# Optimization experiments

Hardware: AMD Instinct MI355X
Metric: run time of the kernel (lower is better)

The kernel has to match this reference:

```python
import jax, jax.numpy as jnp
import numpy as np

B, H, W, C = 4, 64, 64, 256
D = C // 8  # out_channels // queries_ratio = 32


def setup_inputs() -> dict:
    key = jax.random.key(0)
    ks = jax.random.split(key, 8)
    s_in = 1.0 / np.sqrt(C)  # he_normal-ish scale for 1x1 convs
    s_d = 1.0 / np.sqrt(D)
    return {
        "x": jax.random.normal(ks[0], (B, H, W, C), dtype=jnp.float32),
        "Wk": jax.random.normal(ks[1], (C, D), dtype=jnp.float32) * s_in,
        "bk": jnp.zeros((D,), dtype=jnp.float32),
        "Wq": jax.random.normal(ks[2], (C, D), dtype=jnp.float32) * s_in,
        "bq": jnp.zeros((D,), dtype=jnp.float32),
        "Wv": jax.random.normal(ks[3], (C, D), dtype=jnp.float32) * s_in,
        "bv": jnp.zeros((D,), dtype=jnp.float32),
        "Wo": jax.random.normal(ks[4], (D, C), dtype=jnp.float32) * s_d,
        "bo": jnp.zeros((C,), dtype=jnp.float32),
        "gamma": jax.random.normal(ks[5], (1,), dtype=jnp.float32) * 0.1,
    }


def reference(x, Wk, bk, Wq, bq, Wv, bv, Wo, bo, gamma):
    b, h, w, c = x.shape
    n = h * w
    xf = x.reshape(b, n, c)  # flatten spatial -> [B, N, C]
    # 1x1 convs == per-position channel matmuls
    k = xf @ Wk + bk  # [B, N, D]
    q = xf @ Wq + bq  # [B, N, D]
    v = xf @ Wv + bv  # [B, N, D]
    energy = jnp.einsum('bnd,bmd->bnm', q, k)  # [B, N, N] (no scaling, as in source)
    attn = jax.nn.softmax(energy, axis=-1)
    feat = jnp.einsum('bnm,bmd->bnd', attn, v)  # [B, N, D]
    out = feat @ Wo + bo  # 1x1 output conv -> [B, N, C]
    out = gamma[0] * out + xf  # gamma scale + identity shortcut (C_in == C_out)
    return out.reshape(b, h, w, c)
```

## Files before the change

kernel.cpp:

```cpp
#include <hip/hip_runtime.h>
#include <hip/hip_bf16.h>
#include <hip/hip_fp16.h>


#define BB 4
#define NN 4096
#define CC 256
#define DD 32
#define LOG2E 1.44269504088896340736f
#define THR2 11.0f
#define NROW (BB * NN)
#define KSPLIT 4
#define NCH 8

typedef _Float16 half_t;
typedef _Float16 half2_t __attribute__((ext_vector_type(2)));
typedef _Float16 half4_t __attribute__((ext_vector_type(4)));
typedef _Float16 half8_t __attribute__((ext_vector_type(8)));
typedef float f32x4 __attribute__((ext_vector_type(4)));

#define MFMA_QK(a, b, c) __builtin_amdgcn_mfma_f32_16x16x32_f16(a, b, c, 0, 0, 0)
#define MFMA_PV(a, b, c) __builtin_amdgcn_mfma_f32_16x16x16f16(a, b, c, 0, 0, 0)

static __device__ inline float fexp2(float x) {
#if __has_builtin(__builtin_amdgcn_exp2f)
    return __builtin_amdgcn_exp2f(x);
#else
    return exp2f(x);
#endif
}

__global__ __launch_bounds__(512) void proj_kernel(
    const float* __restrict__ x,
    const float* __restrict__ Wk, const float* __restrict__ bk,
    const float* __restrict__ Wq, const float* __restrict__ bq,
    const float* __restrict__ Wv, const float* __restrict__ bv,
    half_t* __restrict__ k_ws, half_t* __restrict__ q_ws, half_t* __restrict__ vT3)
{
    __shared__ half_t xs16[64][264];
    __shared__ half_t Wt[96][264];

    const int t = threadIdx.x;
    const int xcd = blockIdx.x & 7, slot = blockIdx.x >> 3;
    const int bb = xcd >> 1;
    const int c64 = (slot << 1) | (xcd & 1);
    const int row0 = bb * NN + c64 * 64;

    const float4* x4 = reinterpret_cast<const float4*>(x) + (size_t)row0 * 64;
    for (int idx = t; idx < 64 * 64; idx += 512) {
        int r = idx >> 6, c4 = idx & 63;
        float4 v = x4[r * 64 + c4];
        half4_t h;
        h[0] = (half_t)v.x; h[1] = (half_t)v.y; h[2] = (half_t)v.z; h[3] = (half_t)v.w;
        *reinterpret_cast<half4_t*>(&xs16[r][c4 * 4]) = h;
    }

    for (int idx = t; idx < 3072; idx += 512) {
        int cp = idx & 127;
        int rest = idx >> 7;
        int d4 = (rest & 7) * 4;
        int mat = rest >> 3;
        const float* Wm = (mat == 0) ? Wk : ((mat == 1) ? Wq : Wv);
        const float sc = (mat == 1) ? LOG2E : 1.0f;
        float4 w0 = *reinterpret_cast<const float4*>(Wm + (2 * cp) * DD + d4);
        float4 w1 = *reinterpret_cast<const float4*>(Wm + (2 * cp + 1) * DD + d4);
        int rbase = mat * 32 + d4;
        half2_t h;
        h[0] = (half_t)(w0.x * sc); h[1] = (half_t)(w1.x * sc);
        *reinterpret_cast<half2_t*>(&Wt[rbase + 0][2 * cp]) = h;
        h[0] = (half_t)(w0.y * sc); h[1] = (half_t)(w1.y * sc);
        *reinterpret_cast<half2_t*>(&Wt[rbase + 1][2 * cp]) = h;
        h[0] = (half_t)(w0.z * sc); h[1] = (half_t)(w1.z * sc);
        *reinterpret_cast<half2_t*>(&Wt[rbase + 2][2 * cp]) = h;
        h[0] = (half_t)(w0.w * sc); h[1] = (half_t)(w1.w * sc);
        *reinterpret_cast<half2_t*>(&Wt[rbase + 3][2 * cp]) = h;
    }
    __syncthreads();

    const int w = t >> 6, lane = t & 63;
    const int c = lane & 15, g = lane >> 4;
    const int rt = w >> 1;
    const int ct0 = (w & 1) * 3;

    f32x4 acc[3];
#pragma unroll
    for (int j = 0; j < 3; ++j) acc[j] = (f32x4){0.f, 0.f, 0.f, 0.f};

#pragma unroll
    for (int kk = 0; kk < 8; ++kk) {
        const int k0 = kk * 32 + g * 8;
        half8_t bfrag = *reinterpret_cast<const half8_t*>(&xs16[rt * 16 + c][k0]);
#pragma unroll
        for (int j = 0; j < 3; ++j) {
            half8_t afrag = *reinterpret_cast<const half8_t*>(&Wt[(ct0 + j) * 16 + c][k0]);
            acc[j] = MFMA_QK(afrag, bfrag, acc[j]);
        }
    }

    const int grow = row0 + rt * 16 + c;
#pragma unroll
    for (int j = 0; j < 3; ++j) {
        const int ct = ct0 + j;
        const int mat = ct >> 1;
        const float* bm = (mat == 0) ? bk : ((mat == 1) ? bq : bv);
        float4 bb4 = *reinterpret_cast<const float4*>(bm + (ct & 1) * 16 + g * 4);
        const int d0 = (ct & 1) * 16 + g * 4;
        if (mat < 2) {
            const float bsc = (mat == 1) ? LOG2E : 1.0f;
            half_t* dst = (mat == 0) ? k_ws : q_ws;
            half4_t h;
            h[0] = (half_t)(acc[j][0] + bb4.x * bsc);
            h[1] = (half_t)(acc[j][1] + bb4.y * bsc);
            h[2] = (half_t)(acc[j][2] + bb4.z * bsc);
            h[3] = (half_t)(acc[j][3] + bb4.w * bsc);
            *reinterpret_cast<half4_t*>(dst + (size_t)grow * DD + d0) = h;
        } else {
            const size_t tbase = (size_t)(grow >> 4) * 512;
            float vals[4] = {acc[j][0] + bb4.x, acc[j][1] + bb4.y,
                             acc[j][2] + bb4.z, acc[j][3] + bb4.w};
#pragma unroll
            for (int i = 0; i < 4; ++i) {
                int d = d0 + i;
                int l = ((c >> 2) << 4) | (d & 15);
                int h = l * 8 + ((d >> 4) << 2) + (c & 3);
                vT3[tbase + h] = (half_t)vals[i];
            }
        }
    }
}

__global__ __launch_bounds__(512) void attn_partial(
    const half_t* __restrict__ k_ws, const half_t* __restrict__ q_ws,
    const half_t* __restrict__ vT3,
    float* __restrict__ pm, float* __restrict__ ps, float* __restrict__ pO)
{
    __shared__ half_t kbuf[2][8][512];
    __shared__ half_t vbuf[2][8][512];

    const int tid = threadIdx.x;
    const int w = tid >> 6, lane = tid & 63;
    const int q = lane & 15, g = lane >> 4;
    const int xcd = blockIdx.x & 7, rest = blockIdx.x >> 3;
    const int b = xcd >> 1;
    const int u = (rest << 1) | (xcd & 1);
    const int qu = u >> 2;
    const int ks = u & 3;
    const int r0 = b * NN + qu * 256;

    half8_t qf0 = *reinterpret_cast<const half8_t*>(
        q_ws + (size_t)(r0 + (2 * w + 0) * 16 + q) * DD + g * 8);
    half8_t qf1 = *reinterpret_cast<const half8_t*>(
        q_ws + (size_t)(r0 + (2 * w + 1) * 16 + q) * DD + g * 8);

    float m0 = -3.0e38f, m1 = -3.0e38f, ss0 = 0.f, ss1 = 0.f;
    f32x4 acc00 = {0.f, 0.f, 0.f, 0.f};
    f32x4 acc01 = {0.f, 0.f, 0.f, 0.f};
    f32x4 acc10 = {0.f, 0.f, 0.f, 0.f};
    f32x4 acc11 = {0.f, 0.f, 0.f, 0.f};

    const int t0 = ks * 64;
    const half_t* ksrc = k_ws + ((size_t)b * NN + q) * DD + g * 8;
    const half_t* vsrc = vT3 + (size_t)lane * 8;

    {
        half8_t sK = *reinterpret_cast<const half8_t*>(ksrc + (size_t)(t0 + w) * 16 * DD);
        half8_t sV = *reinterpret_cast<const half8_t*>(vsrc + (size_t)(b * 256 + t0 + w) * 512);
        *reinterpret_cast<half8_t*>(&kbuf[0][w][lane * 8]) = sK;
        *reinterpret_cast<half8_t*>(&vbuf[0][w][lane * 8]) = sV;
    }
    __syncthreads();

    for (int ch = 0; ch < NCH; ++ch) {
        const int cb = ch & 1;

        half8_t sK, sV;
        if (ch + 1 < NCH) {
            const int lt = t0 + (ch + 1) * 8 + w;
            sK = *reinterpret_cast<const half8_t*>(ksrc + (size_t)lt * 16 * DD);
            sV = *reinterpret_cast<const half8_t*>(vsrc + (size_t)(b * 256 + lt) * 512);
        }

#pragma unroll
        for (int t = 0; t < 8; ++t) {
            half8_t kf = *reinterpret_cast<const half8_t*>(&kbuf[cb][t][lane * 8]);
            half8_t vv = *reinterpret_cast<const half8_t*>(&vbuf[cb][t][lane * 8]);

            f32x4 z = {0.f, 0.f, 0.f, 0.f};
            f32x4 sA = MFMA_QK(kf, qf0, z);
            f32x4 sB = MFMA_QK(kf, qf1, z);

            float tA = fmaxf(fmaxf(sA[0], sA[1]), fmaxf(sA[2], sA[3]));
            float tB = fmaxf(fmaxf(sB[0], sB[1]), fmaxf(sB[2], sB[3]));
            bool need = (tA > m0 + THR2) || (tB > m1 + THR2);
            if (__any(need)) {
                float rA = fmaxf(tA, __shfl_xor(tA, 16));
                rA = fmaxf(rA, __shfl_xor(rA, 32));
                float rB = fmaxf(tB, __shfl_xor(tB, 16));
                rB = fmaxf(rB, __shfl_xor(rB, 32));
                float n0 = fmaxf(m0, rA), n1 = fmaxf(m1, rB);
                float c0 = fexp2(m0 - n0), c1 = fexp2(m1 - n1);
                ss0 *= c0; ss1 *= c1;
                acc00 *= c0; acc01 *= c0;
                acc10 *= c1; acc11 *= c1;
                m0 = n0; m1 = n1;
            }

            float pA0 = fexp2(sA[0] - m0), pA1 = fexp2(sA[1] - m0);
            float pA2 = fexp2(sA[2] - m0), pA3 = fexp2(sA[3] - m0);
            float pB0 = fexp2(sB[0] - m1), pB1 = fexp2(sB[1] - m1);
            float pB2 = fexp2(sB[2] - m1), pB3 = fexp2(sB[3] - m1);
            ss0 += (pA0 + pA1) + (pA2 + pA3);
            ss1 += (pB0 + pB1) + (pB2 + pB3);

            half4_t pf0, pf1;
            pf0[0] = (half_t)pA0; pf0[1] = (half_t)pA1; pf0[2] = (half_t)pA2; pf0[3] = (half_t)pA3;
            pf1[0] = (half_t)pB0; pf1[1] = (half_t)pB1; pf1[2] = (half_t)pB2; pf1[3] = (half_t)pB3;

            half4_t va0 = __builtin_shufflevector(vv, vv, 0, 1, 2, 3);
            half4_t va1 = __builtin_shufflevector(vv, vv, 4, 5, 6, 7);

            acc00 = MFMA_PV(va0, pf0, acc00);
            acc01 = MFMA_PV(va1, pf0, acc01);
            acc10 = MFMA_PV(va0, pf1, acc10);
            acc11 = MFMA_PV(va1, pf1, acc11);
        }

        if (ch + 1 < NCH) {
            *reinterpret_cast<half8_t*>(&kbuf[cb ^ 1][w][lane * 8]) = sK;
            *reinterpret_cast<half8_t*>(&vbuf[cb ^ 1][w][lane * 8]) = sV;
        }
        __syncthreads();
    }

    ss0 += __shfl_xor(ss0, 16);
    ss0 += __shfl_xor(ss0, 32);
    ss1 += __shfl_xor(ss1, 16);
    ss1 += __shfl_xor(ss1, 32);

    if (lane < 16) {
        pm[(size_t)ks * NROW + r0 + (2 * w + 0) * 16 + lane] = m0;
        ps[(size_t)ks * NROW + r0 + (2 * w + 0) * 16 + lane] = ss0;
        pm[(size_t)ks * NROW + r0 + (2 * w + 1) * 16 + lane] = m1;
        ps[(size_t)ks * NROW + r0 + (2 * w + 1) * 16 + lane] = ss1;
    }
    {
        const int rA = r0 + (2 * w + 0) * 16 + q;
        float* po = pO + ((size_t)ks * NROW + rA) * 32;
        *reinterpret_cast<f32x4*>(po + g * 4) = acc00;
        *reinterpret_cast<f32x4*>(po + 16 + g * 4) = acc01;
    }
    {
        const int rB = r0 + (2 * w + 1) * 16 + q;
        float* po = pO + ((size_t)ks * NROW + rB) * 32;
        *reinterpret_cast<f32x4*>(po + g * 4) = acc10;
        *reinterpret_cast<f32x4*>(po + 16 + g * 4) = acc11;
    }
}

__global__ __launch_bounds__(512) void attn_combine(
    const float* __restrict__ pm, const float* __restrict__ ps,
    const float* __restrict__ pO,
    const float* __restrict__ x, const float* __restrict__ Wo,
    const float* __restrict__ bo, const float* __restrict__ gamma,
    float* __restrict__ out)
{
    __shared__ half_t feat_h[64 * 40];
    __shared__ half_t woT[256 * 40];

    const int tid = threadIdx.x;
    const int b = blockIdx.x >> 6, qb = blockIdx.x & 63;
    const int q0 = qb * 64;
    const int r0 = b * NN + q0;

#pragma unroll
    for (int it = 0; it < 16; ++it) {
        int idx = tid + it * 512;
        int c = idx & 255, d = idx >> 8;
        woT[c * 40 + d] = (half_t)Wo[d * CC + c];
    }

    {
        const int r = tid >> 3, d4 = (tid & 7) * 4;
        const int gr = r0 + r;
        float mv[4];
        float M = -3.0e38f;
#pragma unroll
        for (int k = 0; k < KSPLIT; ++k) {
            mv[k] = pm[(size_t)k * NROW + gr];
            M = fmaxf(M, mv[k]);
        }
        float S = 0.f;
        f32x4 f = {0.f, 0.f, 0.f, 0.f};
#pragma unroll
        for (int k = 0; k < KSPLIT; ++k) {
            float wgt = fexp2(mv[k] - M);
            S += ps[(size_t)k * NROW + gr] * wgt;
            f32x4 p = *reinterpret_cast<const f32x4*>(pO + ((size_t)k * NROW + gr) * 32 + d4);
            f += p * wgt;
        }
        float inv = 1.0f / S;
#pragma unroll
        for (int i = 0; i < 4; ++i) feat_h[r * 40 + d4 + i] = (half_t)(f[i] * inv);
    }
    __syncthreads();

    const int w = tid >> 6, lane = tid & 63;
    const int q = lane & 15, g = lane >> 4;
    const float gam = gamma[0];
#pragma unroll
    for (int j = 0; j < 2; ++j) {
        const int ct = w * 2 + j;
        half8_t kfe = *reinterpret_cast<const half8_t*>(&woT[(ct * 16 + q) * 40 + g * 8]);
        float4 bb4 = *reinterpret_cast<const float4*>(bo + ct * 16 + g * 4);
#pragma unroll
        for (int rt = 0; rt < 4; ++rt) {
            half8_t qfe = *reinterpret_cast<const half8_t*>(&feat_h[(rt * 16 + q) * 40 + g * 8]);
            f32x4 z = {0.f, 0.f, 0.f, 0.f};
            f32x4 o = MFMA_QK(kfe, qfe, z);
            const size_t base = ((size_t)b * NN + q0 + rt * 16 + q) * CC + ct * 16 + g * 4;
            float4 xv = *reinterpret_cast<const float4*>(x + base);
            float4 ov;
            ov.x = gam * (o[0] + bb4.x) + xv.x;
            ov.y = gam * (o[1] + bb4.y) + xv.y;
            ov.z = gam * (o[2] + bb4.z) + xv.z;
            ov.w = gam * (o[3] + bb4.w) + xv.w;
            *reinterpret_cast<float4*>(out + base) = ov;
        }
    }
}

extern "C" void kernel_launch(void* const* d_in, const int* in_sizes, int n_in,
                              void* d_out, int out_size, void* d_ws, size_t ws_size,
                              hipStream_t stream) {
    const float* x  = (const float*)d_in[0];
    const float* Wk = (const float*)d_in[1];
    const float* bk = (const float*)d_in[2];
    const float* Wq = (const float*)d_in[3];
    const float* bq = (const float*)d_in[4];
    const float* Wv = (const float*)d_in[5];
    const float* bv = (const float*)d_in[6];
    const float* Wo = (const float*)d_in[7];
    const float* bo = (const float*)d_in[8];
    const float* gamma = (const float*)d_in[9];
    float* out = (float*)d_out;

    half_t* k_ws = (half_t*)d_ws;
    half_t* q_ws = k_ws + (size_t)BB * NN * DD;
    half_t* vT3  = q_ws + (size_t)BB * NN * DD;
    float*  pm   = (float*)(vT3 + (size_t)BB * NN * DD);
    float*  ps   = pm + (size_t)KSPLIT * NROW;
    float*  pO   = ps + (size_t)KSPLIT * NROW;

    proj_kernel<<<256, 512, 0, stream>>>(x, Wk, bk, Wq, bq, Wv, bv, k_ws, q_ws, vT3);
    attn_partial<<<256, 512, 0, stream>>>(k_ws, q_ws, vT3, pm, ps, pO);
    attn_combine<<<256, 512, 0, stream>>>(pm, ps, pO, x, Wo, bo, gamma, out);
}
```

Before: 45.67 us.

## Halve query rows per attention block and double grid size

Each wave of attn_partial now handles one 16-row query tile instead of two, so a block covers 128 query rows and the grid doubles to 512 blocks. The intent is more parallelism and lower register pressure, giving more waves in flight across the CUs. The cost is that every K/V tile staged in LDS now feeds half as many queries, so K/V global loads and LDS traffic per unit of work double. Probability conversion to fp16 also switches to the packed round-toward-zero cvt_pkrtz instruction.

```diff
diff --git a/kernel.cpp b/kernel.cpp
--- a/kernel.cpp
+++ b/kernel.cpp
@@ -28,6 +28,11 @@
 #else
     return exp2f(x);
 #endif
+}
+
+static __device__ __forceinline__ half2_t pk_f16(float a, float b) {
+    auto r = __builtin_amdgcn_cvt_pkrtz(a, b);
+    return *reinterpret_cast<half2_t*>(&r);
 }
 
 __global__ __launch_bounds__(512) void proj_kernel(
@@ -143,20 +148,16 @@
     const int xcd = blockIdx.x & 7, rest = blockIdx.x >> 3;
     const int b = xcd >> 1;
     const int u = (rest << 1) | (xcd & 1);
-    const int qu = u >> 2;
+    const int qb = u >> 2;
     const int ks = u & 3;
-    const int r0 = b * NN + qu * 256;
-
-    half8_t qf0 = *reinterpret_cast<const half8_t*>(
-        q_ws + (size_t)(r0 + (2 * w + 0) * 16 + q) * DD + g * 8);
-    half8_t qf1 = *reinterpret_cast<const half8_t*>(
-        q_ws + (size_t)(r0 + (2 * w + 1) * 16 + q) * DD + g * 8);
-
-    float m0 = -3.0e38f, m1 = -3.0e38f, ss0 = 0.f, ss1 = 0.f;
-    f32x4 acc00 = {0.f, 0.f, 0.f, 0.f};
-    f32x4 acc01 = {0.f, 0.f, 0.f, 0.f};
-    f32x4 acc10 = {0.f, 0.f, 0.f, 0.f};
-    f32x4 acc11 = {0.f, 0.f, 0.f, 0.f};
+    const int r0 = b * NN + qb * 128;
+
+    half8_t qf = *reinterpret_cast<const half8_t*>(
+        q_ws + (size_t)(r0 + w * 16 + q) * DD + g * 8);
+
+    float m = -3.0e38f, ss = 0.f;
+    f32x4 acc0 = {0.f, 0.f, 0.f, 0.f};
+    f32x4 acc1 = {0.f, 0.f, 0.f, 0.f};
 
     const int t0 = ks * 64;
     const half_t* ksrc = k_ws + ((size_t)b * NN + q) * DD + g * 8;
@@ -186,43 +187,34 @@
             half8_t vv = *reinterpret_cast<const half8_t*>(&vbuf[cb][t][lane * 8]);
 
             f32x4 z = {0.f, 0.f, 0.f, 0.f};
-            f32x4 sA = MFMA_QK(kf, qf0, z);
-            f32x4 sB = MFMA_QK(kf, qf1, z);
-
-            float tA = fmaxf(fmaxf(sA[0], sA[1]), fmaxf(sA[2], sA[3]));
-            float tB = fmaxf(fmaxf(sB[0], sB[1]), fmaxf(sB[2], sB[3]));
-            bool need = (tA > m0 + THR2) || (tB > m1 + THR2);
-            if (__any(need)) {
-                float rA = fmaxf(tA, __shfl_xor(tA, 16));
-                rA = fmaxf(rA, __shfl_xor(rA, 32));
-                float rB = fmaxf(tB, __shfl_xor(tB, 16));
-                rB = fmaxf(rB, __shfl_xor(rB, 32));
-                float n0 = fmaxf(m0, rA), n1 = fmaxf(m1, rB);
-                float c0 = fexp2(m0 - n0), c1 = fexp2(m1 - n1);
-                ss0 *= c0; ss1 *= c1;
-                acc00 *= c0; acc01 *= c0;
-                acc10 *= c1; acc11 *= c1;
-                m0 = n0; m1 = n1;
+            f32x4 s = MFMA_QK(kf, qf, z);
+
+            float tmax = fmaxf(fmaxf(s[0], s[1]), fmaxf(s[2], s[3]));
+            if (!__all(tmax <= m + THR2)) {
+                float rmax = fmaxf(tmax, __shfl_xor(tmax, 16));
+                rmax = fmaxf(rmax, __shfl_xor(rmax, 32));
+                float mn = fmaxf(m, rmax);
+                float sc = fexp2(m - mn);
+                ss *= sc;
+                acc0 *= sc;
+                acc1 *= sc;
+                m = mn;
             }
 
-            float pA0 = fexp2(sA[0] - m0), pA1 = fexp2(sA[1] - m0);
-            float pA2 = fexp2(sA[2] - m0), pA3 = fexp2(sA[3] - m0);
-            float pB0 = fexp2(sB[0] - m1), pB1 = fexp2(sB[1] - m1);
-            float pB2 = fexp2(sB[2] - m1), pB3 = fexp2(sB[3] - m1);
-            ss0 += (pA0 + pA1) + (pA2 + pA3);
-            ss1 += (pB0 + pB1) + (pB2 + pB3);
-
-            half4_t pf0, pf1;
-            pf0[0] = (half_t)pA0; pf0[1] = (half_t)pA1; pf0[2] = (half_t)pA2; pf0[3] = (half_t)pA3;
-            pf1[0] = (half_t)pB0; pf1[1] = (half_t)pB1; pf1[2] = (half_t)pB2; pf1[3] = (half_t)pB3;
+            float p0 = fexp2(s[0] - m), p1 = fexp2(s[1] - m);
+            float p2 = fexp2(s[2] - m), p3 = fexp2(s[3] - m);
+            ss += (p0 + p1) + (p2 + p3);
+
+            half2_t pa = pk_f16(p0, p1);
+            half2_t pb = pk_f16(p2, p3);
+            half4_t pf;
+            pf[0] = pa[0]; pf[1] = pa[1]; pf[2] = pb[0]; pf[3] = pb[1];
 
             half4_t va0 = __builtin_shufflevector(vv, vv, 0, 1, 2, 3);
             half4_t va1 = __builtin_shufflevector(vv, vv, 4, 5, 6, 7);
 
-            acc00 = MFMA_PV(va0, pf0, acc00);
-            acc01 = MFMA_PV(va1, pf0, acc01);
-            acc10 = MFMA_PV(va0, pf1, acc10);
-            acc11 = MFMA_PV(va1, pf1, acc11);
+            acc0 = MFMA_PV(va0, pf, acc0);
+            acc1 = MFMA_PV(va1, pf, acc1);
         }
 
         if (ch + 1 < NCH) {
@@ -232,28 +224,18 @@
         __syncthreads();
     }
 
-    ss0 += __shfl_xor(ss0, 16);
-    ss0 += __shfl_xor(ss0, 32);
-    ss1 += __shfl_xor(ss1, 16);
-    ss1 += __shfl_xor(ss1, 32);
+    ss += __shfl_xor(ss, 16);
+    ss += __shfl_xor(ss, 32);
 
     if (lane < 16) {
-        pm[(size_t)ks * NROW + r0 + (2 * w + 0) * 16 + lane] = m0;
-        ps[(size_t)ks * NROW + r0 + (2 * w + 0) * 16 + lane] = ss0;
-        pm[(size_t)ks * NROW + r0 + (2 * w + 1) * 16 + lane] = m1;
-        ps[(size_t)ks * NROW + r0 + (2 * w + 1) * 16 + lane] = ss1;
+        pm[(size_t)ks * NROW + r0 + w * 16 + lane] = m;
+        ps[(size_t)ks * NROW + r0 + w * 16 + lane] = ss;
     }
     {
-        const int rA = r0 + (2 * w + 0) * 16 + q;
-        float* po = pO + ((size_t)ks * NROW + rA) * 32;
-        *reinterpret_cast<f32x4*>(po + g * 4) = acc00;
-        *reinterpret_cast<f32x4*>(po + 16 + g * 4) = acc01;
-    }
-    {
-        const int rB = r0 + (2 * w + 1) * 16 + q;
-        float* po = pO + ((size_t)ks * NROW + rB) * 32;
-        *reinterpret_cast<f32x4*>(po + g * 4) = acc10;
-        *reinterpret_cast<f32x4*>(po + 16 + g * 4) = acc11;
+        const int r = r0 + w * 16 + q;
+        float* po = pO + ((size_t)ks * NROW + r) * 32;
+        *reinterpret_cast<f32x4*>(po + g * 4) = acc0;
+        *reinterpret_cast<f32x4*>(po + 16 + g * 4) = acc1;
     }
 }
 
@@ -352,6 +334,6 @@
     float*  pO   = ps + (size_t)KSPLIT * NROW;
 
     proj_kernel<<<256, 512, 0, stream>>>(x, Wk, bk, Wq, bq, Wv, bv, k_ws, q_ws, vT3);
-    attn_partial<<<256, 512, 0, stream>>>(k_ws, q_ws, vT3, pm, ps, pO);
+    attn_partial<<<512, 512, 0, stream>>>(k_ws, q_ws, vT3, pm, ps, pO);
     attn_combine<<<256, 512, 0, stream>>>(pm, ps, pO, x, Wo, bo, gamma, out);
 }
```

Result: faster. 44.31 us (-3.0%).
